# Optimization experiments

Hardware: AMD Instinct MI355X
Metric: run time of the kernel (lower is better)

## Reference

```python
import jax, jax.numpy as jnp
import numpy as np

N_NODES = 50000

def setup_inputs() -> dict:
    key = jax.random.key(0)
    ks = jax.random.split(key, 8)
    d_in, d_h = 128, 128
    x = jax.random.normal(ks[0], (N_NODES, d_in), dtype=jnp.float32)
    edge_index = jax.random.randint(ks[1], (2, 800000), 0, N_NODES, dtype=jnp.int64)
    edge_pairs = jax.random.randint(ks[2], (1000000, 2), 0, N_NODES, dtype=jnp.int64)
    W_gcn = jax.random.normal(ks[3], (d_in, d_h), dtype=jnp.float32) / np.sqrt(d_in)
    b_gcn = jnp.zeros((d_h,), dtype=jnp.float32)
    W1 = jax.random.normal(ks[4], (2 * d_h, d_h), dtype=jnp.float32) / np.sqrt(2 * d_h)
    b1 = jnp.zeros((d_h,), dtype=jnp.float32)
    W2 = jax.random.normal(ks[5], (d_h, 1), dtype=jnp.float32) / np.sqrt(d_h)
    b2 = jnp.zeros((1,), dtype=jnp.float32)
    return {"x": x, "edge_index": edge_index, "edge_pairs": edge_pairs,
            "W_gcn": W_gcn, "b_gcn": b_gcn, "W1": W1, "b1": b1, "W2": W2, "b2": b2}

def gcn_conv(x, edge_index, W, b):
    # PyG GCNConv default: add self-loops, symmetric normalization.
    n = x.shape[0]
    loop = jnp.arange(n, dtype=edge_index.dtype)
    src = jnp.concatenate([edge_index[0], loop])  # [E+N]
    dst = jnp.concatenate([edge_index[1], loop])
    deg = jax.ops.segment_sum(jnp.ones(src.shape[0], dtype=x.dtype), dst, num_segments=n)
    dinv = jnp.where(deg > 0, jax.lax.rsqrt(deg), 0.0)
    norm = dinv[src] * dinv[dst]                  # [E+N]
    h = x @ W                                     # [N, H]
    agg = jax.ops.segment_sum(h[src] * norm[:, None], dst, num_segments=n)
    return agg + b

def reference(x, edge_index, edge_pairs, W_gcn, b_gcn, W1, b1, W2, b2):
    h = gcn_conv(x, edge_index, W_gcn, b_gcn)      # [N, H]
    e = jnp.concatenate([h[edge_pairs[:, 0]], h[edge_pairs[:, 1]]], axis=-1)  # [P, 2H]
    edge_logits = jax.nn.relu(e @ W1 + b1) @ W2 + b2  # [P, 1]
    return edge_logits, edge_pairs, h
```

## Files before the change

kernel.cpp:

```cpp
#include <hip/hip_runtime.h>
#include <hip/hip_fp16.h>

#define WG 256

typedef _Float16 f16;
typedef _Float16 hv2 __attribute__((ext_vector_type(2)));
typedef _Float16 f16x4 __attribute__((ext_vector_type(4)));
typedef _Float16 f16x8 __attribute__((ext_vector_type(8)));
typedef float f32x4 __attribute__((ext_vector_type(4)));

__global__ __launch_bounds__(WG) void k_deg_count(const int* __restrict__ dst,
                                                  int* __restrict__ deg,
                                                  int* __restrict__ rank, int e) {
    int i = blockIdx.x * WG + threadIdx.x;
    if (i < e) rank[i] = atomicAdd(&deg[dst[i]], 1);
}

__global__ __launch_bounds__(WG) void k_scan1(const int* __restrict__ deg,
                                              float* __restrict__ dinv,
                                              int* __restrict__ base,
                                              int* __restrict__ bsum, int n) {
    __shared__ int t[WG];
    int tid = threadIdx.x;
    int i = blockIdx.x * WG + tid;
    int v = (i < n) ? deg[i] : 0;
    if (i < n) dinv[i] = rsqrtf((float)(v + 1));
    t[tid] = v;
    __syncthreads();
    for (int o = 1; o < WG; o <<= 1) {
        int add = (tid >= o) ? t[tid - o] : 0;
        __syncthreads();
        t[tid] += add;
        __syncthreads();
    }
    if (i < n) base[i] = t[tid] - v;
    if (tid == WG - 1) bsum[blockIdx.x] = t[WG - 1];
}

__global__ __launch_bounds__(WG) void k_scan23(int* __restrict__ base,
                                               const int* __restrict__ bsum,
                                               int n, int e, int nb) {
    __shared__ int t[WG];
    int tid = threadIdx.x;
    int v = (tid < nb) ? bsum[tid] : 0;
    t[tid] = v;
    __syncthreads();
    for (int o = 1; o < WG; o <<= 1) {
        int add = (tid >= o) ? t[tid - o] : 0;
        __syncthreads();
        t[tid] += add;
        __syncthreads();
    }
    int off = t[blockIdx.x] - ((blockIdx.x < nb) ? bsum[blockIdx.x] : 0);
    int i = blockIdx.x * WG + tid;
    if (i < n) {
        base[i] += off;
        if (i == n - 1) base[n] = e;
    }
}

__global__ __launch_bounds__(WG) void k_fill(const int* __restrict__ src,
                                             const int* __restrict__ dst,
                                             const int* __restrict__ base,
                                             const int* __restrict__ rank,
                                             int* __restrict__ esrc, int e) {
    int i = blockIdx.x * WG + threadIdx.x;
    if (i >= e) return;
    esrc[base[dst[i]] + rank[i]] = src[i];
}

__global__ __launch_bounds__(WG) void k_misc(const float* __restrict__ Wg,
                                             f16* __restrict__ Wgt,
                                             const float* __restrict__ W1,
                                             f16* __restrict__ W1t,
                                             const int* __restrict__ pairs,
                                             float* __restrict__ outp, int n4) {
    int b = blockIdx.x;
    if (b < 64) {
        int i = b * WG + threadIdx.x;
        int k = i & 127, nI = i >> 7;
        Wgt[i] = (f16)Wg[(size_t)k * 128 + nI];
    } else if (b < 192) {
        int i = (b - 64) * WG + threadIdx.x;
        int k = i & 255, nI = i >> 8;
        W1t[i] = (f16)W1[(size_t)k * 128 + nI];
    } else {
        int i = (b - 192) * WG + threadIdx.x;
        if (i < n4) {
            int4 v = ((const int4*)pairs)[i];
            ((float4*)outp)[i] = make_float4((float)v.x, (float)v.y, (float)v.z, (float)v.w);
        }
    }
}

__global__ __launch_bounds__(WG) void k_mm_hpk(const float* __restrict__ A,
                                               const f16* __restrict__ Wt,
                                               const float* __restrict__ dinv,
                                               __half2* __restrict__ Out, int n) {
    __shared__ f16 As[64][136];
    __shared__ f16 Bs[128][136];
    const int tid = threadIdx.x;
    const int row0 = blockIdx.x * 64;
    for (int f = tid; f < 128 * 16; f += WG) {
        int r = f >> 4, c = f & 15;
        *(float4*)&Bs[r][c * 8] = ((const float4*)Wt)[r * 16 + c];
    }
    for (int f = tid; f < 64 * 32; f += WG) {
        int r = f >> 5, c = f & 31;
        float4 v = make_float4(0.f, 0.f, 0.f, 0.f);
        if (row0 + r < n) v = ((const float4*)A)[(size_t)(row0 + r) * 32 + c];
        *(f16x4*)&As[r][c * 4] = (f16x4){(f16)v.x, (f16)v.y, (f16)v.z, (f16)v.w};
    }
    __syncthreads();
    const int wv = tid >> 6, lane = tid & 63, m = lane & 15, quad = lane >> 4;
    f32x4 acc[8];
#pragma unroll
    for (int t = 0; t < 8; ++t) acc[t] = (f32x4){0.f, 0.f, 0.f, 0.f};
#pragma unroll
    for (int kk = 0; kk < 4; ++kk) {
        f16x8 af = *(f16x8*)&As[wv * 16 + m][kk * 32 + quad * 8];
#pragma unroll
        for (int t = 0; t < 8; ++t) {
            f16x8 bf = *(f16x8*)&Bs[t * 16 + m][kk * 32 + quad * 8];
            acc[t] = __builtin_amdgcn_mfma_f32_16x16x32_f16(af, bf, acc[t], 0, 0, 0);
        }
    }
#pragma unroll
    for (int r = 0; r < 4; ++r) {
        int row = row0 + wv * 16 + quad * 4 + r;
        if (row < n) {
            float dv = dinv[row];
#pragma unroll
            for (int t = 0; t < 4; ++t)
                Out[(size_t)row * 64 + t * 16 + m] =
                    __floats2half2_rn(acc[t][r] * dv, acc[t + 4][r] * dv);
        }
    }
}

__global__ __launch_bounds__(WG) void k_mm_uv(const float* __restrict__ A,
                                              const f16* __restrict__ W1t,
                                              const float* __restrict__ b1,
                                              __half2* __restrict__ Up,
                                              __half2* __restrict__ Vp, int n) {
    __shared__ f16 As[64][136];
    __shared__ f16 Bs[128][136];
    const int tid = threadIdx.x;
    const int row0 = blockIdx.x * 64;
    for (int f = tid; f < 64 * 32; f += WG) {
        int r = f >> 5, c = f & 31;
        float4 v = make_float4(0.f, 0.f, 0.f, 0.f);
        if (row0 + r < n) v = ((const float4*)A)[(size_t)(row0 + r) * 32 + c];
        *(f16x4*)&As[r][c * 4] = (f16x4){(f16)v.x, (f16)v.y, (f16)v.z, (f16)v.w};
    }
    const int wv = tid >> 6, lane = tid & 63, m = lane & 15, quad = lane >> 4;
    f32x4 acc[8];
#pragma unroll
    for (int ph = 0; ph < 2; ++ph) {
        if (ph) __syncthreads();
        for (int f = tid; f < 128 * 16; f += WG) {
            int r = f >> 4, c = f & 15;
            *(float4*)&Bs[r][c * 8] = *(const float4*)(W1t + (size_t)r * 256 + ph * 128 + c * 8);
        }
        __syncthreads();
#pragma unroll
        for (int t = 0; t < 8; ++t) acc[t] = (f32x4){0.f, 0.f, 0.f, 0.f};
#pragma unroll
        for (int kk = 0; kk < 4; ++kk) {
            f16x8 af = *(f16x8*)&As[wv * 16 + m][kk * 32 + quad * 8];
#pragma unroll
            for (int t = 0; t < 8; ++t) {
                f16x8 bf = *(f16x8*)&Bs[t * 16 + m][kk * 32 + quad * 8];
                acc[t] = __builtin_amdgcn_mfma_f32_16x16x32_f16(af, bf, acc[t], 0, 0, 0);
            }
        }
        __half2* Out = ph ? Vp : Up;
#pragma unroll
        for (int t = 0; t < 4; ++t) {
            float bl = 0.f, bh = 0.f;
            if (!ph) { bl = b1[t * 16 + m]; bh = b1[t * 16 + m + 64]; }
#pragma unroll
            for (int r = 0; r < 4; ++r) {
                int row = row0 + wv * 16 + quad * 4 + r;
                if (row < n)
                    Out[(size_t)row * 64 + t * 16 + m] =
                        __floats2half2_rn(acc[t][r] + bl, acc[t + 4][r] + bh);
            }
        }
    }
}

__global__ __launch_bounds__(WG) void k_gather(const __half2* __restrict__ Hpk,
                                               const float* __restrict__ dinv,
                                               const float* __restrict__ bg,
                                               const int* __restrict__ base,
                                               const int* __restrict__ esrc,
                                               float* __restrict__ outh, int n) {
    int tid = threadIdx.x;
    int node = blockIdx.x * 16 + (tid >> 4);
    int sub = tid & 15;
    if (node >= n) return;
    int4 hh = *(const int4*)(Hpk + (size_t)node * 64 + 4 * sub);
    const int* hp = (const int*)&hh;
    float accl[4], acch[4];
#pragma unroll
    for (int k = 0; k < 4; ++k) {
        hv2 h = __builtin_bit_cast(hv2, hp[k]);
        accl[k] = (float)h[0];
        acch[k] = (float)h[1];
    }
    int j = base[node], jend = base[node + 1];
    for (; j + 4 <= jend; j += 4) {
        int s0 = esrc[j], s1 = esrc[j + 1], s2i = esrc[j + 2], s3 = esrc[j + 3];
        int4 r0 = *(const int4*)(Hpk + (size_t)s0 * 64 + 4 * sub);
        int4 r1 = *(const int4*)(Hpk + (size_t)s1 * 64 + 4 * sub);
        int4 r2 = *(const int4*)(Hpk + (size_t)s2i * 64 + 4 * sub);
        int4 r3 = *(const int4*)(Hpk + (size_t)s3 * 64 + 4 * sub);
        const int* p0 = (const int*)&r0;
        const int* p1 = (const int*)&r1;
        const int* p2 = (const int*)&r2;
        const int* p3 = (const int*)&r3;
#pragma unroll
        for (int k = 0; k < 4; ++k) {
            hv2 h0 = __builtin_bit_cast(hv2, p0[k]);
            hv2 h1 = __builtin_bit_cast(hv2, p1[k]);
            hv2 h2 = __builtin_bit_cast(hv2, p2[k]);
            hv2 h3 = __builtin_bit_cast(hv2, p3[k]);
            accl[k] += (float)h0[0] + (float)h1[0] + (float)h2[0] + (float)h3[0];
            acch[k] += (float)h0[1] + (float)h1[1] + (float)h2[1] + (float)h3[1];
        }
    }
    for (; j < jend; ++j) {
        int s = esrc[j];
        int4 r = *(const int4*)(Hpk + (size_t)s * 64 + 4 * sub);
        const int* pr = (const int*)&r;
#pragma unroll
        for (int k = 0; k < 4; ++k) {
            hv2 h = __builtin_bit_cast(hv2, pr[k]);
            accl[k] += (float)h[0];
            acch[k] += (float)h[1];
        }
    }
    float dv = dinv[node];
    float4 blo = *(const float4*)(bg + 4 * sub);
    float4 bhi = *(const float4*)(bg + 4 * sub + 64);
    *(float4*)&outh[(size_t)node * 128 + 4 * sub] =
        make_float4(fmaf(accl[0], dv, blo.x), fmaf(accl[1], dv, blo.y),
                    fmaf(accl[2], dv, blo.z), fmaf(accl[3], dv, blo.w));
    *(float4*)&outh[(size_t)node * 128 + 64 + 4 * sub] =
        make_float4(fmaf(acch[0], dv, bhi.x), fmaf(acch[1], dv, bhi.y),
                    fmaf(acch[2], dv, bhi.z), fmaf(acch[3], dv, bhi.w));
}

__global__ __launch_bounds__(WG) void k_pair8(const __half2* __restrict__ U,
                                              const __half2* __restrict__ V,
                                              const float* __restrict__ W2,
                                              const float* __restrict__ b2,
                                              const int* __restrict__ pairs,
                                              float* __restrict__ out_logit, int p) {
    int wv = (blockIdx.x * WG + threadIdx.x) >> 6;
    int lane = threadIdx.x & 63;
    int g = lane >> 4, sub = lane & 15;
    int q0 = wv * 8 + g, q1 = q0 + 4;
    bool v0 = (q0 < p), v1 = (q1 < p);
    if (!v0) return;
    int qa0 = q0, qa1 = v1 ? q1 : q0;
    int a0 = pairs[2 * qa0], b0 = pairs[2 * qa0 + 1];
    int a1 = pairs[2 * qa1], b1i = pairs[2 * qa1 + 1];

    float4 w2lo = ((const float4*)W2)[sub];
    float4 w2hi = ((const float4*)(W2 + 64))[sub];
    hv2 w2h[4];
    w2h[0] = hv2{(f16)w2lo.x, (f16)w2hi.x};
    w2h[1] = hv2{(f16)w2lo.y, (f16)w2hi.y};
    w2h[2] = hv2{(f16)w2lo.z, (f16)w2hi.z};
    w2h[3] = hv2{(f16)w2lo.w, (f16)w2hi.w};

    int4 u0 = *(const int4*)(U + (size_t)a0 * 64 + 4 * sub);
    int4 vv0 = *(const int4*)(V + (size_t)b0 * 64 + 4 * sub);
    int4 u1 = *(const int4*)(U + (size_t)a1 * 64 + 4 * sub);
    int4 vv1 = *(const int4*)(V + (size_t)b1i * 64 + 4 * sub);
    const int* ui0 = (const int*)&u0;
    const int* vi0 = (const int*)&vv0;
    const int* ui1 = (const int*)&u1;
    const int* vi1 = (const int*)&vv1;

    const hv2 z2 = hv2{(f16)0.f, (f16)0.f};
    float p0 = 0.f, p1 = 0.f;
#pragma unroll
    for (int k = 0; k < 4; ++k) {
        hv2 s0 = __builtin_bit_cast(hv2, ui0[k]) + __builtin_bit_cast(hv2, vi0[k]);
        hv2 s1 = __builtin_bit_cast(hv2, ui1[k]) + __builtin_bit_cast(hv2, vi1[k]);
        p0 = __builtin_amdgcn_fdot2(__builtin_elementwise_max(s0, z2), w2h[k], p0, false);
        p1 = __builtin_amdgcn_fdot2(__builtin_elementwise_max(s1, z2), w2h[k], p1, false);
    }
#pragma unroll
    for (int m = 1; m < 16; m <<= 1) {
        p0 += __shfl_xor(p0, m, 64);
        p1 += __shfl_xor(p1, m, 64);
    }
    if (sub == 0) {
        float bb = b2[0];
        out_logit[q0] = p0 + bb;
        if (v1) out_logit[q1] = p1 + bb;
    }
}

extern "C" void kernel_launch(void* const* d_in, const int* in_sizes, int n_in,
                              void* d_out, int out_size, void* d_ws, size_t ws_size,
                              hipStream_t stream) {
    const float* x     = (const float*)d_in[0];
    const int*   eidx  = (const int*)d_in[1];
    const int*   pairs = (const int*)d_in[2];
    const float* W_gcn = (const float*)d_in[3];
    const float* b_gcn = (const float*)d_in[4];
    const float* W1    = (const float*)d_in[5];
    const float* b1    = (const float*)d_in[6];
    const float* W2    = (const float*)d_in[7];
    const float* b2    = (const float*)d_in[8];

    const int N = in_sizes[0] / 128;
    const int E = in_sizes[1] / 2;
    const int P = in_sizes[2] / 2;
    const int* esrc_in = eidx;
    const int* edst_in = eidx + E;

    float* ws      = (float*)d_ws;
    int*   deg     = (int*)d_ws;
    float* dinv    = ws + 65536;
    int*   base    = (int*)(ws + 131072);
    int*   bsum    = (int*)(ws + 196608);
    f16*   Wt_gcn  = (f16*)(ws + 197120);
    f16*   W1t     = (f16*)(ws + 205312);
    int*   rank    = (int*)(ws + 221696);
    int*   ecsr    = (int*)(ws + 221696 + (size_t)E);
    __half2* Hpk   = (__half2*)(ws + 221696 + 2 * (size_t)E);
    __half2* Upk   = Hpk + (size_t)N * 64;
    __half2* Vpk   = Upk + (size_t)N * 64;

    float* out_logit = (float*)d_out;
    float* out_pairs = out_logit + P;
    float* out_h     = out_logit + 3 * (size_t)P;

    const int nb = (N + WG - 1) / WG;
    dim3 blk(WG);
    dim3 grid_pair((unsigned)((P + 31) / 32));
    dim3 grid_misc((unsigned)(192 + (P / 2 + WG - 1) / WG));
    hipMemsetAsync(deg, 0, (size_t)N * 4, stream);
    k_deg_count <<<(E + WG - 1) / WG, blk, 0, stream>>>(edst_in, deg, rank, E);
    k_scan1     <<<nb, blk, 0, stream>>>(deg, dinv, base, bsum, N);
    k_scan23    <<<nb, blk, 0, stream>>>(base, bsum, N, E, nb);
    k_fill      <<<(E + WG - 1) / WG, blk, 0, stream>>>(esrc_in, edst_in, base, rank, ecsr, E);
    k_misc      <<<grid_misc, blk, 0, stream>>>(W_gcn, Wt_gcn, W1, W1t, pairs, out_pairs, P / 2);
    k_mm_hpk    <<<(N + 63) / 64, blk, 0, stream>>>(x, Wt_gcn, dinv, Hpk, N);
    k_gather    <<<(N + 15) / 16, blk, 0, stream>>>(Hpk, dinv, b_gcn, base, ecsr, out_h, N);
    k_mm_uv     <<<(N + 63) / 64, blk, 0, stream>>>(out_h, W1t, b1, Upk, Vpk, N);
    k_pair8     <<<grid_pair, blk, 0, stream>>>(Upk, Vpk, W2, b2, pairs, out_logit, P);
}
```

Measured before the change: 277.2 us.

## Fuse CSR build into cooperative kernel and gather into UV matmul

Replaces the memset plus five preprocessing launches (degree count, two scan passes, fill, weight transpose and pair conversion) with one cooperative persistent kernel that uses grid-wide syncs between phases. It also fuses the neighbor aggregation into the UV matmul kernel, so aggregated rows go straight into shared memory as f16 and are not re-read from global memory. This removes several launch gaps and one full read of h. In exchange, the gather now runs with only 64 rows per block, which lowers its parallelism, and the grid syncs add their own cost.

```diff
diff --git a/kernel.cpp b/kernel.cpp
--- a/kernel.cpp
+++ b/kernel.cpp
@@ -1,5 +1,8 @@
 #include <hip/hip_runtime.h>
 #include <hip/hip_fp16.h>
+#include <hip/hip_cooperative_groups.h>
+
+namespace cg = cooperative_groups;
 
 #define WG 256
 
@@ -9,88 +12,82 @@
 typedef _Float16 f16x8 __attribute__((ext_vector_type(8)));
 typedef float f32x4 __attribute__((ext_vector_type(4)));
 
-__global__ __launch_bounds__(WG) void k_deg_count(const int* __restrict__ dst,
-                                                  int* __restrict__ deg,
-                                                  int* __restrict__ rank, int e) {
-    int i = blockIdx.x * WG + threadIdx.x;
-    if (i < e) rank[i] = atomicAdd(&deg[dst[i]], 1);
-}
-
-__global__ __launch_bounds__(WG) void k_scan1(const int* __restrict__ deg,
-                                              float* __restrict__ dinv,
-                                              int* __restrict__ base,
-                                              int* __restrict__ bsum, int n) {
+__global__ __launch_bounds__(WG, 4) void k_csr(const int* __restrict__ src,
+                                               const int* __restrict__ dst,
+                                               int* __restrict__ deg,
+                                               int* __restrict__ rank,
+                                               int* __restrict__ base,
+                                               int* __restrict__ bsum,
+                                               float* __restrict__ dinv,
+                                               const float* __restrict__ Wg,
+                                               f16* __restrict__ Wgt,
+                                               const float* __restrict__ W1,
+                                               f16* __restrict__ W1t,
+                                               const int* __restrict__ pairs,
+                                               float* __restrict__ outp,
+                                               int* __restrict__ esrc,
+                                               int n, int e, int nb, int p4) {
+    cg::grid_group grid = cg::this_grid();
     __shared__ int t[WG];
-    int tid = threadIdx.x;
-    int i = blockIdx.x * WG + tid;
-    int v = (i < n) ? deg[i] : 0;
-    if (i < n) dinv[i] = rsqrtf((float)(v + 1));
-    t[tid] = v;
-    __syncthreads();
-    for (int o = 1; o < WG; o <<= 1) {
-        int add = (tid >= o) ? t[tid - o] : 0;
-        __syncthreads();
-        t[tid] += add;
-        __syncthreads();
-    }
-    if (i < n) base[i] = t[tid] - v;
-    if (tid == WG - 1) bsum[blockIdx.x] = t[WG - 1];
-}
-
-__global__ __launch_bounds__(WG) void k_scan23(int* __restrict__ base,
-                                               const int* __restrict__ bsum,
-                                               int n, int e, int nb) {
-    __shared__ int t[WG];
-    int tid = threadIdx.x;
-    int v = (tid < nb) ? bsum[tid] : 0;
-    t[tid] = v;
-    __syncthreads();
-    for (int o = 1; o < WG; o <<= 1) {
-        int add = (tid >= o) ? t[tid - o] : 0;
-        __syncthreads();
-        t[tid] += add;
-        __syncthreads();
-    }
-    int off = t[blockIdx.x] - ((blockIdx.x < nb) ? bsum[blockIdx.x] : 0);
-    int i = blockIdx.x * WG + tid;
-    if (i < n) {
-        base[i] += off;
-        if (i == n - 1) base[n] = e;
-    }
-}
-
-__global__ __launch_bounds__(WG) void k_fill(const int* __restrict__ src,
-                                             const int* __restrict__ dst,
-                                             const int* __restrict__ base,
-                                             const int* __restrict__ rank,
-                                             int* __restrict__ esrc, int e) {
-    int i = blockIdx.x * WG + threadIdx.x;
-    if (i >= e) return;
-    esrc[base[dst[i]] + rank[i]] = src[i];
-}
-
-__global__ __launch_bounds__(WG) void k_misc(const float* __restrict__ Wg,
-                                             f16* __restrict__ Wgt,
-                                             const float* __restrict__ W1,
-                                             f16* __restrict__ W1t,
-                                             const int* __restrict__ pairs,
-                                             float* __restrict__ outp, int n4) {
-    int b = blockIdx.x;
-    if (b < 64) {
-        int i = b * WG + threadIdx.x;
+    const int tid = threadIdx.x;
+    const int G = gridDim.x * WG;
+    const int gtid = blockIdx.x * WG + tid;
+
+    for (int i = gtid; i < n; i += G) deg[i] = 0;
+    for (int i = gtid; i < 128 * 128; i += G) {
         int k = i & 127, nI = i >> 7;
         Wgt[i] = (f16)Wg[(size_t)k * 128 + nI];
-    } else if (b < 192) {
-        int i = (b - 64) * WG + threadIdx.x;
+    }
+    for (int i = gtid; i < 128 * 256; i += G) {
         int k = i & 255, nI = i >> 8;
         W1t[i] = (f16)W1[(size_t)k * 128 + nI];
-    } else {
-        int i = (b - 192) * WG + threadIdx.x;
-        if (i < n4) {
-            int4 v = ((const int4*)pairs)[i];
-            ((float4*)outp)[i] = make_float4((float)v.x, (float)v.y, (float)v.z, (float)v.w);
-        }
-    }
+    }
+    for (int i = gtid; i < p4; i += G) {
+        int4 v = ((const int4*)pairs)[i];
+        ((float4*)outp)[i] = make_float4((float)v.x, (float)v.y, (float)v.z, (float)v.w);
+    }
+    grid.sync();
+
+    for (int i = gtid; i < e; i += G) rank[i] = atomicAdd(&deg[dst[i]], 1);
+    grid.sync();
+
+    for (int tile = blockIdx.x; tile < nb; tile += gridDim.x) {
+        int i = tile * WG + tid;
+        int v = (i < n) ? deg[i] : 0;
+        if (i < n) dinv[i] = rsqrtf((float)(v + 1));
+        t[tid] = v;
+        __syncthreads();
+        for (int o = 1; o < WG; o <<= 1) {
+            int add = (tid >= o) ? t[tid - o] : 0;
+            __syncthreads();
+            t[tid] += add;
+            __syncthreads();
+        }
+        if (i < n) base[i] = t[tid] - v;
+        if (tid == WG - 1) bsum[tile] = t[WG - 1];
+        __syncthreads();
+    }
+    grid.sync();
+
+    if (blockIdx.x == 0) {
+        int v = (tid < nb) ? bsum[tid] : 0;
+        t[tid] = v;
+        __syncthreads();
+        for (int o = 1; o < WG; o <<= 1) {
+            int add = (tid >= o) ? t[tid - o] : 0;
+            __syncthreads();
+            t[tid] += add;
+            __syncthreads();
+        }
+        if (tid < nb) bsum[tid] = t[tid] - v;
+    }
+    grid.sync();
+
+    for (int i = gtid; i < n; i += G) base[i] += bsum[i >> 8];
+    if (gtid == 0) base[n] = e;
+    grid.sync();
+
+    for (int i = gtid; i < e; i += G) esrc[base[dst[i]] + rank[i]] = src[i];
 }
 
 __global__ __launch_bounds__(WG) void k_mm_hpk(const float* __restrict__ A,
@@ -138,26 +135,91 @@
     }
 }
 
-__global__ __launch_bounds__(WG) void k_mm_uv(const float* __restrict__ A,
-                                              const f16* __restrict__ W1t,
-                                              const float* __restrict__ b1,
-                                              __half2* __restrict__ Up,
-                                              __half2* __restrict__ Vp, int n) {
+__global__ __launch_bounds__(WG) void k_gather_uv(const __half2* __restrict__ Hpk,
+                                                  const float* __restrict__ dinv,
+                                                  const float* __restrict__ bg,
+                                                  const int* __restrict__ base,
+                                                  const int* __restrict__ esrc,
+                                                  const f16* __restrict__ W1t,
+                                                  const float* __restrict__ b1,
+                                                  float* __restrict__ outh,
+                                                  __half2* __restrict__ Up,
+                                                  __half2* __restrict__ Vp, int n) {
     __shared__ f16 As[64][136];
     __shared__ f16 Bs[128][136];
     const int tid = threadIdx.x;
     const int row0 = blockIdx.x * 64;
-    for (int f = tid; f < 64 * 32; f += WG) {
-        int r = f >> 5, c = f & 31;
-        float4 v = make_float4(0.f, 0.f, 0.f, 0.f);
-        if (row0 + r < n) v = ((const float4*)A)[(size_t)(row0 + r) * 32 + c];
-        *(f16x4*)&As[r][c * 4] = (f16x4){(f16)v.x, (f16)v.y, (f16)v.z, (f16)v.w};
-    }
+    const int sub = tid & 15;
+
+#pragma unroll
+    for (int pass = 0; pass < 4; ++pass) {
+        int r = pass * 16 + (tid >> 4);
+        int node = row0 + r;
+        if (node < n) {
+            int4 hh = *(const int4*)(Hpk + (size_t)node * 64 + 4 * sub);
+            const int* hp = (const int*)&hh;
+            float accl[4], acch[4];
+#pragma unroll
+            for (int k = 0; k < 4; ++k) {
+                hv2 h = __builtin_bit_cast(hv2, hp[k]);
+                accl[k] = (float)h[0];
+                acch[k] = (float)h[1];
+            }
+            int j = base[node], jend = base[node + 1];
+            for (; j + 4 <= jend; j += 4) {
+                int s0 = esrc[j], s1 = esrc[j + 1], s2i = esrc[j + 2], s3 = esrc[j + 3];
+                int4 r0 = *(const int4*)(Hpk + (size_t)s0 * 64 + 4 * sub);
+                int4 r1 = *(const int4*)(Hpk + (size_t)s1 * 64 + 4 * sub);
+                int4 r2 = *(const int4*)(Hpk + (size_t)s2i * 64 + 4 * sub);
+                int4 r3 = *(const int4*)(Hpk + (size_t)s3 * 64 + 4 * sub);
+                const int* p0 = (const int*)&r0;
+                const int* p1 = (const int*)&r1;
+                const int* p2 = (const int*)&r2;
+                const int* p3 = (const int*)&r3;
+#pragma unroll
+                for (int k = 0; k < 4; ++k) {
+                    hv2 h0 = __builtin_bit_cast(hv2, p0[k]);
+                    hv2 h1 = __builtin_bit_cast(hv2, p1[k]);
+                    hv2 h2 = __builtin_bit_cast(hv2, p2[k]);
+                    hv2 h3 = __builtin_bit_cast(hv2, p3[k]);
+                    accl[k] += (float)h0[0] + (float)h1[0] + (float)h2[0] + (float)h3[0];
+                    acch[k] += (float)h0[1] + (float)h1[1] + (float)h2[1] + (float)h3[1];
+                }
+            }
+            for (; j < jend; ++j) {
+                int s = esrc[j];
+                int4 rr = *(const int4*)(Hpk + (size_t)s * 64 + 4 * sub);
+                const int* pr = (const int*)&rr;
+#pragma unroll
+                for (int k = 0; k < 4; ++k) {
+                    hv2 h = __builtin_bit_cast(hv2, pr[k]);
+                    accl[k] += (float)h[0];
+                    acch[k] += (float)h[1];
+                }
+            }
+            float dv = dinv[node];
+            float4 blo = *(const float4*)(bg + 4 * sub);
+            float4 bhi = *(const float4*)(bg + 4 * sub + 64);
+            float ol[4], oh[4];
+#pragma unroll
+            for (int k = 0; k < 4; ++k) {
+                ol[k] = fmaf(accl[k], dv, ((const float*)&blo)[k]);
+                oh[k] = fmaf(acch[k], dv, ((const float*)&bhi)[k]);
+            }
+            *(float4*)&outh[(size_t)node * 128 + 4 * sub] =
+                make_float4(ol[0], ol[1], ol[2], ol[3]);
+            *(float4*)&outh[(size_t)node * 128 + 64 + 4 * sub] =
+                make_float4(oh[0], oh[1], oh[2], oh[3]);
+            *(f16x4*)&As[r][4 * sub] = (f16x4){(f16)ol[0], (f16)ol[1], (f16)ol[2], (f16)ol[3]};
+            *(f16x4*)&As[r][64 + 4 * sub] = (f16x4){(f16)oh[0], (f16)oh[1], (f16)oh[2], (f16)oh[3]};
+        }
+    }
+
     const int wv = tid >> 6, lane = tid & 63, m = lane & 15, quad = lane >> 4;
     f32x4 acc[8];
 #pragma unroll
     for (int ph = 0; ph < 2; ++ph) {
-        if (ph) __syncthreads();
+        __syncthreads();
         for (int f = tid; f < 128 * 16; f += WG) {
             int r = f >> 4, c = f & 15;
             *(float4*)&Bs[r][c * 8] = *(const float4*)(W1t + (size_t)r * 256 + ph * 128 + c * 8);
@@ -188,68 +250,6 @@
             }
         }
     }
-}
-
-__global__ __launch_bounds__(WG) void k_gather(const __half2* __restrict__ Hpk,
-                                               const float* __restrict__ dinv,
-                                               const float* __restrict__ bg,
-                                               const int* __restrict__ base,
-                                               const int* __restrict__ esrc,
-                                               float* __restrict__ outh, int n) {
-    int tid = threadIdx.x;
-    int node = blockIdx.x * 16 + (tid >> 4);
-    int sub = tid & 15;
-    if (node >= n) return;
-    int4 hh = *(const int4*)(Hpk + (size_t)node * 64 + 4 * sub);
-    const int* hp = (const int*)&hh;
-    float accl[4], acch[4];
-#pragma unroll
-    for (int k = 0; k < 4; ++k) {
-        hv2 h = __builtin_bit_cast(hv2, hp[k]);
-        accl[k] = (float)h[0];
-        acch[k] = (float)h[1];
-    }
-    int j = base[node], jend = base[node + 1];
-    for (; j + 4 <= jend; j += 4) {
-        int s0 = esrc[j], s1 = esrc[j + 1], s2i = esrc[j + 2], s3 = esrc[j + 3];
-        int4 r0 = *(const int4*)(Hpk + (size_t)s0 * 64 + 4 * sub);
-        int4 r1 = *(const int4*)(Hpk + (size_t)s1 * 64 + 4 * sub);
-        int4 r2 = *(const int4*)(Hpk + (size_t)s2i * 64 + 4 * sub);
-        int4 r3 = *(const int4*)(Hpk + (size_t)s3 * 64 + 4 * sub);
-        const int* p0 = (const int*)&r0;
-        const int* p1 = (const int*)&r1;
-        const int* p2 = (const int*)&r2;
-        const int* p3 = (const int*)&r3;
-#pragma unroll
-        for (int k = 0; k < 4; ++k) {
-            hv2 h0 = __builtin_bit_cast(hv2, p0[k]);
-            hv2 h1 = __builtin_bit_cast(hv2, p1[k]);
-            hv2 h2 = __builtin_bit_cast(hv2, p2[k]);
-            hv2 h3 = __builtin_bit_cast(hv2, p3[k]);
-            accl[k] += (float)h0[0] + (float)h1[0] + (float)h2[0] + (float)h3[0];
-            acch[k] += (float)h0[1] + (float)h1[1] + (float)h2[1] + (float)h3[1];
-        }
-    }
-    for (; j < jend; ++j) {
-        int s = esrc[j];
-        int4 r = *(const int4*)(Hpk + (size_t)s * 64 + 4 * sub);
-        const int* pr = (const int*)&r;
-#pragma unroll
-        for (int k = 0; k < 4; ++k) {
-            hv2 h = __builtin_bit_cast(hv2, pr[k]);
-            accl[k] += (float)h[0];
-            acch[k] += (float)h[1];
-        }
-    }
-    float dv = dinv[node];
-    float4 blo = *(const float4*)(bg + 4 * sub);
-    float4 bhi = *(const float4*)(bg + 4 * sub + 64);
-    *(float4*)&outh[(size_t)node * 128 + 4 * sub] =
-        make_float4(fmaf(accl[0], dv, blo.x), fmaf(accl[1], dv, blo.y),
-                    fmaf(accl[2], dv, blo.z), fmaf(accl[3], dv, blo.w));
-    *(float4*)&outh[(size_t)node * 128 + 64 + 4 * sub] =
-        make_float4(fmaf(acch[0], dv, bhi.x), fmaf(acch[1], dv, bhi.y),
-                    fmaf(acch[2], dv, bhi.z), fmaf(acch[3], dv, bhi.w));
 }
 
 __global__ __launch_bounds__(WG) void k_pair8(const __half2* __restrict__ U,
@@ -343,17 +343,18 @@
     float* out_h     = out_logit + 3 * (size_t)P;
 
     const int nb = (N + WG - 1) / WG;
+    int nI = N, eI = E, nbI = nb, p4 = P / 2;
+    void* csr_args[] = {
+        (void*)&esrc_in, (void*)&edst_in, (void*)&deg, (void*)&rank, (void*)&base,
+        (void*)&bsum, (void*)&dinv, (void*)&W_gcn, (void*)&Wt_gcn, (void*)&W1,
+        (void*)&W1t, (void*)&pairs, (void*)&out_pairs, (void*)&ecsr,
+        (void*)&nI, (void*)&eI, (void*)&nbI, (void*)&p4};
+    hipLaunchCooperativeKernel((const void*)k_csr, dim3(1024), dim3(WG), csr_args, 0, stream);
+
     dim3 blk(WG);
     dim3 grid_pair((unsigned)((P + 31) / 32));
-    dim3 grid_misc((unsigned)(192 + (P / 2 + WG - 1) / WG));
-    hipMemsetAsync(deg, 0, (size_t)N * 4, stream);
-    k_deg_count <<<(E + WG - 1) / WG, blk, 0, stream>>>(edst_in, deg, rank, E);
-    k_scan1     <<<nb, blk, 0, stream>>>(deg, dinv, base, bsum, N);
-    k_scan23    <<<nb, blk, 0, stream>>>(base, bsum, N, E, nb);
-    k_fill      <<<(E + WG - 1) / WG, blk, 0, stream>>>(esrc_in, edst_in, base, rank, ecsr, E);
-    k_misc      <<<grid_misc, blk, 0, stream>>>(W_gcn, Wt_gcn, W1, W1t, pairs, out_pairs, P / 2);
-    k_mm_hpk    <<<(N + 63) / 64, blk, 0, stream>>>(x, Wt_gcn, dinv, Hpk, N);
-    k_gather    <<<(N + 15) / 16, blk, 0, stream>>>(Hpk, dinv, b_gcn, base, ecsr, out_h, N);
-    k_mm_uv     <<<(N + 63) / 64, blk, 0, stream>>>(out_h, W1t, b1, Upk, Vpk, N);
-    k_pair8     <<<grid_pair, blk, 0, stream>>>(Upk, Vpk, W2, b2, pairs, out_logit, P);
-}
+    k_mm_hpk   <<<(N + 63) / 64, blk, 0, stream>>>(x, Wt_gcn, dinv, Hpk, N);
+    k_gather_uv<<<(N + 63) / 64, blk, 0, stream>>>(Hpk, dinv, b_gcn, base, ecsr, W1t, b1,
+                                                   out_h, Upk, Vpk, N);
+    k_pair8    <<<grid_pair, blk, 0, stream>>>(Upk, Vpk, W2, b2, pairs, out_logit, P);
+}
```

Result: slower. 811.9 us (+192.9%).
